# Performance work log

Measured on AMD Instinct MI355X. Metric: run time of the kernel, lower is better.

## Reference

```python
import jax, jax.numpy as jnp
import numpy as np

N = 100000   # nodes
E = 1600000  # edges
IN = 128     # in_dim
H = 64       # hidden_dim
EPS = 1e-5


def layer_norm(x, g, b):
    mu = x.mean(-1, keepdims=True)
    v = ((x - mu) ** 2).mean(-1, keepdims=True)
    return (x - mu) * jax.lax.rsqrt(v + EPS) * g + b


def gcn_conv(x, W, b, src, dst, dinv):
    # PyG GCNConv: x' = D^{-1/2}(A+I)D^{-1/2} X W + b (degrees include self-loops)
    h = x @ W                                   # [N, H]
    coef = dinv[src] * dinv[dst]                # [E]
    agg = jax.ops.segment_sum(h[src] * coef[:, None], dst, num_segments=N)
    agg = agg + h * (dinv * dinv)[:, None]      # self-loop term
    return agg + b


def setup_inputs() -> dict:
    key = jax.random.key(0)
    ks = jax.random.split(key, 12)
    inp = {
        "x": jax.random.normal(ks[0], (N, IN), jnp.float32),
        "edge_index": jax.random.randint(ks[1], (2, E), 0, N, dtype=jnp.int64
                                         if jax.config.jax_enable_x64 else jnp.int32),
    }
    dims = [(IN, H), (H, H), (H, H)]
    for i, (di, do) in enumerate(dims, start=1):
        inp[f"W{i}"] = jax.random.normal(ks[2 * i], (di, do), jnp.float32) / np.sqrt(di)
        inp[f"b{i}"] = jnp.zeros((do,), jnp.float32)
        inp[f"g{i}"] = jnp.ones((do,), jnp.float32)
        inp[f"be{i}"] = jnp.zeros((do,), jnp.float32)
    inp["Wh"] = jax.random.normal(ks[11], (H, 1), jnp.float32) / np.sqrt(H)
    inp["bh"] = jnp.zeros((1,), jnp.float32)
    return inp


def reference(x, edge_index, W1, b1, g1, be1, W2, b2, g2, be2, W3, b3, g3, be3, Wh, bh):
    src, dst = edge_index[0], edge_index[1]
    deg = jax.ops.segment_sum(jnp.ones((E,), x.dtype), dst, num_segments=N) + 1.0
    dinv = jax.lax.rsqrt(deg)
    for W, b, g, be in ((W1, b1, g1, be1), (W2, b2, g2, be2), (W3, b3, g3, be3)):
        x = gcn_conv(x, W, b, src, dst, dinv)
        x = layer_norm(x, g, be)
        x = jax.nn.gelu(x, approximate=False)  # F.gelu default = exact erf
        # dropout omitted (eval mode / deterministic reference)
    return (x @ Wh + bh).squeeze(-1)  # [N]
```

## Files before the change

### kernel.cpp

```cpp
#include <hip/hip_runtime.h>
#include <math.h>

#define NODES 100000
#define EDGES 1600000
#define NBUCK 196
#define BCAP2 12288
#define EPB 4096
#define BINB 391
#define GEMMB 1563

typedef __attribute__((ext_vector_type(8))) short short8;
typedef __attribute__((ext_vector_type(4))) float floatx4;
typedef __attribute__((ext_vector_type(4))) unsigned uv4;

__device__ __forceinline__ float gsum8(float x) {
#pragma unroll
  for (int o = 4; o > 0; o >>= 1) x += __shfl_xor(x, o, 64);
  return x;
}

__device__ __forceinline__ short f2bf(float f) {
  union { float f; unsigned u; } v;
  v.f = f;
  unsigned r = 0x7fffu + ((v.u >> 16) & 1u);
  return (short)((v.u + r) >> 16);
}
__device__ __forceinline__ float bflo(unsigned p) {
  union { unsigned u; float f; } v; v.u = p << 16; return v.f;
}
__device__ __forceinline__ float bfhi(unsigned p) {
  union { unsigned u; float f; } v; v.u = p & 0xffff0000u; return v.f;
}

#define BIN_SMEM (4 * 256 * 4 + EPB * 4 + EPB)
__device__ __forceinline__ void bin_body(char* smemraw, int b, const int* __restrict__ src,
                                         const int* __restrict__ dst, int* __restrict__ bins,
                                         int* __restrict__ gcur) {
  int* cnt = (int*)smemraw;
  int* gb = cnt + 256;
  int* lb = gb + 256;
  int* lcur = lb + 256;
  int* rec = lcur + 256;
  unsigned char* rbk = (unsigned char*)(rec + EPB);
  int t = threadIdx.x;
  cnt[t] = 0;
  __syncthreads();
  int base = b * EPB;
  int nv = EDGES - base; if (nv > EPB) nv = EPB;
  int s[16], d[16];
#pragma unroll
  for (int j = 0; j < 16; ++j) {
    int e = base + j * 256 + t;
    if (e < EDGES) {
      s[j] = src[e];
      d[j] = dst[e];
      atomicAdd(&cnt[d[j] >> 9], 1);
    } else {
      d[j] = -1;
    }
  }
  __syncthreads();
  int c = cnt[t];
  lb[t] = c;
  __syncthreads();
  for (int o = 1; o < 256; o <<= 1) {
    int u = (t >= o) ? lb[t - o] : 0;
    __syncthreads();
    lb[t] += u;
    __syncthreads();
  }
  int ex = lb[t] - c;
  gb[t] = (c > 0) ? atomicAdd(&gcur[t], c) : 0;
  __syncthreads();
  lb[t] = ex;
  lcur[t] = ex;
  __syncthreads();
#pragma unroll
  for (int j = 0; j < 16; ++j) {
    if (d[j] >= 0) {
      int bk = d[j] >> 9;
      int lp = atomicAdd(&lcur[bk], 1);
      rec[lp] = s[j] | ((d[j] & 511) << 17);
      rbk[lp] = (unsigned char)bk;
    }
  }
  __syncthreads();
  for (int i = t; i < nv; i += 256) {
    int bk = rbk[i];
    int pos = gb[bk] + (i - lb[bk]);
    if (pos < BCAP2) bins[bk * BCAP2 + pos] = rec[i];
  }
}

#define FILL_SMEM (256 * 4 + 512 * 4 + 512 * 4 + 4 * 4 + BCAP2 * 4)
__device__ __forceinline__ void fill_body(char* smemraw, int b, const int* __restrict__ bins,
                                          const int* __restrict__ gcur, int* __restrict__ rowptr,
                                          float* __restrict__ dinv, int* __restrict__ csr) {
  int* bsm = (int*)smemraw;
  int* cnt = bsm + 256;
  int* cur = cnt + 512;
  int* wtot = cur + 512;
  int* stage = wtot + 4;
  int t = threadIdx.x;
  int v = 0;
  if (t < NBUCK) { v = gcur[t]; if (v > BCAP2) v = BCAP2; }
  bsm[t] = v;
  cnt[t] = 0; cnt[t + 256] = 0;
  __syncthreads();
  for (int o = 1; o < 256; o <<= 1) {
    int u = (t >= o) ? bsm[t - o] : 0;
    __syncthreads();
    bsm[t] += u;
    __syncthreads();
  }
  if (b == 0 && t == NBUCK - 1) rowptr[NODES] = bsm[t];
  int cb = gcur[b]; if (cb > BCAP2) cb = BCAP2;
  int bbase = bsm[b] - cb;
  const int* bp = &bins[(size_t)b * BCAP2];
  for (int i = t; i < cb; i += 256)
    atomicAdd(&cnt[(bp[i] >> 17) & 511], 1);
  __syncthreads();
  int a0 = cnt[2 * t], a1 = cnt[2 * t + 1];
  int sum2 = a0 + a1;
  int lane = t & 63, w = t >> 6;
  int inc = sum2;
#pragma unroll
  for (int o = 1; o < 64; o <<= 1) {
    int u = __shfl_up(inc, o, 64);
    if (lane >= o) inc += u;
  }
  if (lane == 63) wtot[w] = inc;
  __syncthreads();
  int wpre = 0;
  for (int ww = 0; ww < w; ++ww) wpre += wtot[ww];
  int l0 = wpre + inc - sum2;
  int l1 = l0 + a0;
  int n0 = b * 512 + 2 * t, n1 = n0 + 1;
  if (n0 < NODES) { rowptr[n0] = bbase + l0; dinv[n0] = rsqrtf((float)a0 + 1.0f); }
  if (n1 < NODES) { rowptr[n1] = bbase + l1; dinv[n1] = rsqrtf((float)a1 + 1.0f); }
  cur[2 * t] = l0; cur[2 * t + 1] = l1;
  __syncthreads();
  for (int i = t; i < cb; i += 256) {
    int pk = bp[i];
    int lp = atomicAdd(&cur[(pk >> 17) & 511], 1);
    stage[lp] = pk & 0x1FFFF;
  }
  __syncthreads();
  for (int i = t; i < cb; i += 256) csr[bbase + i] = stage[i];
}

#define GEMM_SMEM (64 * 136 * 2)
__device__ __forceinline__ void gemm_body(char* smemraw, int tile0, const float* __restrict__ x,
                                          const float* __restrict__ W, short* __restrict__ hs) {
  constexpr int K = 128, KP = K + 8;
  short* wt = (short*)smemraw;
  for (int idx = threadIdx.x; idx < K * 64; idx += 256) {
    int k = idx >> 6, n = idx & 63;
    wt[n * KP + k] = f2bf(W[idx]);
  }
  __syncthreads();
  int wid = threadIdx.x >> 6, lane = threadIdx.x & 63;
  int tile = tile0 + wid;
  if (tile * 16 >= NODES) return;
  int m = lane & 15, q = lane >> 4;

  short8 bfr[4][K / 32];
#pragma unroll
  for (int ct = 0; ct < 4; ++ct)
#pragma unroll
    for (int ks = 0; ks < K / 32; ++ks)
      bfr[ct][ks] = *reinterpret_cast<const short8*>(&wt[(ct * 16 + m) * KP + ks * 32 + q * 8]);

  floatx4 acc[4];
#pragma unroll
  for (int ct = 0; ct < 4; ++ct) acc[ct] = {0.f, 0.f, 0.f, 0.f};
  int r0 = tile * 16;
#pragma unroll
  for (int ks = 0; ks < K / 32; ++ks) {
    const float* xp = &x[(size_t)(r0 + m) * K + ks * 32 + q * 8];
    floatx4 a0 = *reinterpret_cast<const floatx4*>(xp);
    floatx4 a1 = *reinterpret_cast<const floatx4*>(xp + 4);
    short8 af;
#pragma unroll
    for (int j = 0; j < 4; ++j) { af[j] = f2bf(a0[j]); af[4 + j] = f2bf(a1[j]); }
#pragma unroll
    for (int ct = 0; ct < 4; ++ct)
      acc[ct] = __builtin_amdgcn_mfma_f32_16x16x32_bf16(af, bfr[ct][ks], acc[ct], 0, 0, 0);
  }
#pragma unroll
  for (int ct = 0; ct < 4; ++ct)
#pragma unroll
    for (int r = 0; r < 4; ++r) {
      int row = r0 + q * 4 + r, col = ct * 16 + m;
      hs[row * 64 + col] = f2bf(acc[ct][r]);
    }
}

template <bool PRESCALED>
__device__ __forceinline__ void do_agg(const uv4* __restrict__ hsv, const float* __restrict__ dinv,
                                       const int* __restrict__ csr, int n, int e0, int e1,
                                       int lane, float dn, float acc[8]) {
  int q = lane & 7, srcb = lane & 0x38;
  uv4 sv = hsv[(size_t)n * 8 + q];
#pragma unroll
  for (int w = 0; w < 4; ++w) {
    float lo = bflo(sv[w]), hi = bfhi(sv[w]);
    if constexpr (PRESCALED) { acc[2 * w] = lo; acc[2 * w + 1] = hi; }
    else { acc[2 * w] = lo * dn; acc[2 * w + 1] = hi * dn; }
  }
  for (int base = e0; base < e1; base += 8) {
    int cnt = e1 - base;
    if (cnt > 8) cnt = 8;
    int a = base + (q < cnt ? q : 0);
    int sidx = csr[a];
    float gq = 1.0f;
    if constexpr (!PRESCALED) gq = dinv[sidx];
    int s[8]; float wj[8];
#pragma unroll
    for (int j = 0; j < 8; ++j) {
      s[j] = __shfl(sidx, srcb | j, 64);
      if constexpr (!PRESCALED) {
        float bj = __shfl(gq, srcb | j, 64);
        wj[j] = (j < cnt) ? bj : 0.0f;
      } else {
        wj[j] = 1.0f;
      }
    }
    uv4 v[8];
#pragma unroll
    for (int j = 0; j < 8; ++j) v[j] = hsv[(size_t)s[j] * 8 + q];
    if constexpr (PRESCALED) {
      if (cnt == 8) {
#pragma unroll
        for (int j = 0; j < 8; ++j)
#pragma unroll
          for (int w = 0; w < 4; ++w) { acc[2 * w] += bflo(v[j][w]); acc[2 * w + 1] += bfhi(v[j][w]); }
      } else {
#pragma unroll
        for (int j = 0; j < 8; ++j)
          if (j < cnt)
#pragma unroll
            for (int w = 0; w < 4; ++w) { acc[2 * w] += bflo(v[j][w]); acc[2 * w + 1] += bfhi(v[j][w]); }
      }
    } else {
#pragma unroll
      for (int j = 0; j < 8; ++j)
#pragma unroll
        for (int w = 0; w < 4; ++w) {
          acc[2 * w]     += wj[j] * bflo(v[j][w]);
          acc[2 * w + 1] += wj[j] * bfhi(v[j][w]);
        }
    }
  }
}

template <bool PRESCALED>
__global__ __launch_bounds__(256) void k_aggg(const short* __restrict__ hs,
                                              const float* __restrict__ dinv,
                                              const int* __restrict__ rowptr,
                                              const int* __restrict__ csr,
                                              const float* __restrict__ bias,
                                              const float* __restrict__ gam,
                                              const float* __restrict__ bet,
                                              const float* __restrict__ W,
                                              short* __restrict__ hsn) {
  __shared__ __align__(16) short wt[64 * 72];
  __shared__ __align__(16) short ut[32 * 72];
  int t = threadIdx.x;
  for (int idx = t; idx < 4096; idx += 256) {
    int k = idx >> 6, n = idx & 63;
    wt[n * 72 + k] = f2bf(W[idx]);
  }
  const uv4* hsv = (const uv4*)hs;
  int lane = t & 63, wid = t >> 6;
  int g = lane >> 3, q = lane & 7;
  int nb0 = blockIdx.x * 32;
  int r = wid * 8 + g;
  int n = nb0 + r;
  int e0 = rowptr[n], e1 = rowptr[n + 1];
  float dn = dinv[n];
  float acc[8];
  do_agg<PRESCALED>(hsv, dinv, csr, n, e0, e1, lane, dn, acc);

  const floatx4* bi4 = (const floatx4*)bias;
  floatx4 b0 = bi4[q * 2], b1 = bi4[q * 2 + 1];
#pragma unroll
  for (int f = 0; f < 4; ++f) { acc[f] = acc[f] * dn + b0[f]; acc[f + 4] = acc[f + 4] * dn + b1[f]; }

  float lsum = 0.f;
#pragma unroll
  for (int f = 0; f < 8; ++f) lsum += acc[f];
  float mu = gsum8(lsum) * (1.0f / 64.0f);
  float d[8], lvar = 0.f;
#pragma unroll
  for (int f = 0; f < 8; ++f) { d[f] = acc[f] - mu; lvar += d[f] * d[f]; }
  float rs = rsqrtf(gsum8(lvar) * (1.0f / 64.0f) + 1e-5f);
  const floatx4* gm4 = (const floatx4*)gam;
  const floatx4* bt4 = (const floatx4*)bet;
  floatx4 g0 = gm4[q * 2], g1 = gm4[q * 2 + 1];
  floatx4 t0 = bt4[q * 2], t1 = bt4[q * 2 + 1];
  short8 us;
#pragma unroll
  for (int f = 0; f < 8; ++f) {
    float gv = (f < 4) ? g0[f] : g1[f - 4];
    float tv = (f < 4) ? t0[f] : t1[f - 4];
    float vv = d[f] * rs * gv + tv;
    float u = 0.5f * vv * (1.0f + erff(vv * 0.70710678118654752f));
    us[f] = f2bf(u * dn);
  }
  *reinterpret_cast<short8*>(&ut[r * 72 + q * 8]) = us;
  __syncthreads();

  int m = lane & 15, q2 = lane >> 4;
  int tile = wid >> 1, cb = (wid & 1) * 2;
  short8 bfr[2][2];
#pragma unroll
  for (int ct = 0; ct < 2; ++ct)
#pragma unroll
    for (int ks = 0; ks < 2; ++ks)
      bfr[ct][ks] = *reinterpret_cast<const short8*>(&wt[((cb + ct) * 16 + m) * 72 + ks * 32 + q2 * 8]);
  floatx4 ac[2];
#pragma unroll
  for (int ct = 0; ct < 2; ++ct) ac[ct] = {0.f, 0.f, 0.f, 0.f};
#pragma unroll
  for (int ks = 0; ks < 2; ++ks) {
    short8 af = *reinterpret_cast<const short8*>(&ut[(tile * 16 + m) * 72 + ks * 32 + q2 * 8]);
#pragma unroll
    for (int ct = 0; ct < 2; ++ct)
      ac[ct] = __builtin_amdgcn_mfma_f32_16x16x32_bf16(af, bfr[ct][ks], ac[ct], 0, 0, 0);
  }
#pragma unroll
  for (int ct = 0; ct < 2; ++ct)
#pragma unroll
    for (int rr = 0; rr < 4; ++rr) {
      int row = nb0 + tile * 16 + q2 * 4 + rr, col = (cb + ct) * 16 + m;
      hsn[row * 64 + col] = f2bf(ac[ct][rr]);
    }
}

__global__ __launch_bounds__(256) void k_agg_fin(const short* __restrict__ hs,
                                                 const float* __restrict__ dinv,
                                                 const int* __restrict__ rowptr,
                                                 const int* __restrict__ csr,
                                                 const float* __restrict__ bias,
                                                 const float* __restrict__ gam,
                                                 const float* __restrict__ bet,
                                                 const float* __restrict__ Wh,
                                                 const float* __restrict__ bh,
                                                 float* __restrict__ out) {
  const uv4* hsv = (const uv4*)hs;
  int lane = threadIdx.x & 63, wid = threadIdx.x >> 6;
  int g = lane >> 3, q = lane & 7;
  int n = blockIdx.x * 32 + wid * 8 + g;
  int e0 = rowptr[n], e1 = rowptr[n + 1];
  float dn = dinv[n];
  float acc[8];
  do_agg<true>(hsv, dinv, csr, n, e0, e1, lane, dn, acc);
  const floatx4* bi4 = (const floatx4*)bias;
  floatx4 b0 = bi4[q * 2], b1 = bi4[q * 2 + 1];
#pragma unroll
  for (int f = 0; f < 4; ++f) { acc[f] = acc[f] * dn + b0[f]; acc[f + 4] = acc[f + 4] * dn + b1[f]; }
  float lsum = 0.f;
#pragma unroll
  for (int f = 0; f < 8; ++f) lsum += acc[f];
  float mu = gsum8(lsum) * (1.0f / 64.0f);
  float d[8], lvar = 0.f;
#pragma unroll
  for (int f = 0; f < 8; ++f) { d[f] = acc[f] - mu; lvar += d[f] * d[f]; }
  float rs = rsqrtf(gsum8(lvar) * (1.0f / 64.0f) + 1e-5f);
  const floatx4* gm4 = (const floatx4*)gam;
  const floatx4* bt4 = (const floatx4*)bet;
  floatx4 g0 = gm4[q * 2], g1 = gm4[q * 2 + 1];
  floatx4 t0 = bt4[q * 2], t1 = bt4[q * 2 + 1];
  const floatx4* wh4 = (const floatx4*)Wh;
  floatx4 w0 = wh4[q * 2], w1 = wh4[q * 2 + 1];
  float lp = 0.f;
#pragma unroll
  for (int f = 0; f < 8; ++f) {
    float gv = (f < 4) ? g0[f] : g1[f - 4];
    float tv = (f < 4) ? t0[f] : t1[f - 4];
    float wv = (f < 4) ? w0[f] : w1[f - 4];
    float vv = d[f] * rs * gv + tv;
    float u = 0.5f * vv * (1.0f + erff(vv * 0.70710678118654752f));
    lp += u * wv;
  }
  float p = gsum8(lp);
  if (q == 0) out[n] = p + bh[0];
}

__global__ __launch_bounds__(256) void k_pre1(const int* __restrict__ src, const int* __restrict__ dst,
                                              int* __restrict__ bins, int* __restrict__ gcur,
                                              const float* __restrict__ x, const float* __restrict__ W1,
                                              short* __restrict__ hs) {
  __shared__ __align__(16) char smem[BIN_SMEM];
  int b = blockIdx.x;
  if (b < BINB) bin_body(smem, b, src, dst, bins, gcur);
  else gemm_body(smem, (b - BINB) * 4, x, W1, hs);
}

__global__ __launch_bounds__(256) void k_pre2(const int* __restrict__ bins, const int* __restrict__ gcur,
                                              int* __restrict__ rowptr, float* __restrict__ dinv,
                                              int* __restrict__ csr) {
  __shared__ __align__(16) char smem[FILL_SMEM];
  fill_body(smem, blockIdx.x, bins, gcur, rowptr, dinv, csr);
}

__global__ __launch_bounds__(256) void k_bin2(const int* src, const int* dst, int* bins, int* gcur) {
  __shared__ __align__(16) char smem[BIN_SMEM];
  bin_body(smem, blockIdx.x, src, dst, bins, gcur);
}
__global__ __launch_bounds__(256) void k_fillb2(const int* bins, const int* gcur, int* rowptr,
                                                float* dinv, int* csr) {
  __shared__ __align__(16) char smem[FILL_SMEM];
  fill_body(smem, blockIdx.x, bins, gcur, rowptr, dinv, csr);
}
__global__ __launch_bounds__(256) void k_gemm(const float* x, const float* W, short* hs) {
  __shared__ __align__(16) char smem[GEMM_SMEM];
  gemm_body(smem, blockIdx.x * 4, x, W, hs);
}

extern "C" void kernel_launch(void* const* d_in, const int* in_sizes, int n_in,
                              void* d_out, int out_size, void* d_ws, size_t ws_size,
                              hipStream_t stream) {
  const float* x  = (const float*)d_in[0];
  const int* ei   = (const int*)d_in[1];
  const float* W1 = (const float*)d_in[2];
  const float* b1 = (const float*)d_in[3];
  const float* g1 = (const float*)d_in[4];
  const float* be1= (const float*)d_in[5];
  const float* W2 = (const float*)d_in[6];
  const float* b2 = (const float*)d_in[7];
  const float* g2 = (const float*)d_in[8];
  const float* be2= (const float*)d_in[9];
  const float* W3 = (const float*)d_in[10];
  const float* b3 = (const float*)d_in[11];
  const float* g3 = (const float*)d_in[12];
  const float* be3= (const float*)d_in[13];
  const float* Wh = (const float*)d_in[14];
  const float* bh = (const float*)d_in[15];
  const int* srcp = ei;
  const int* dstp = ei + EDGES;

  char* ws = (char*)d_ws;
  size_t off = 0;
  auto take = [&](size_t bytes) {
    char* p = ws + off;
    off = (off + bytes + 255) & ~(size_t)255;
    return p;
  };
  float* dinv = (float*)take((size_t)NODES * 4);
  int* rowptr = (int*)take((size_t)(NODES + 1) * 4);
  int* csr    = (int*)take((size_t)EDGES * 4);
  short* hs_a = (short*)take((size_t)NODES * 64 * 2);
  short* hs_b = (short*)take((size_t)NODES * 64 * 2);

  size_t bins_sz = (size_t)NBUCK * BCAP2 * 4;
  bool overlap = (ws_size >= off + bins_sz + 4096);
  int* bins; int* gcur;
  if (overlap) {
    bins = (int*)take(bins_sz);
    gcur = (int*)take((size_t)NBUCK * 4);
  } else {
    bins = (int*)hs_a;
    gcur = (int*)hs_b;
  }

  (void)hipMemsetAsync(gcur, 0, (size_t)NBUCK * 4, stream);
  if (overlap) {
    k_pre1<<<BINB + GEMMB, 256, 0, stream>>>(srcp, dstp, bins, gcur, x, W1, hs_a);
    k_pre2<<<NBUCK, 256, 0, stream>>>(bins, gcur, rowptr, dinv, csr);
  } else {
    k_bin2<<<BINB, 256, 0, stream>>>(srcp, dstp, bins, gcur);
    k_fillb2<<<NBUCK, 256, 0, stream>>>(bins, gcur, rowptr, dinv, csr);
    k_gemm<<<GEMMB, 256, 0, stream>>>(x, W1, hs_a);
  }
  k_aggg<false><<<NODES / 32, 256, 0, stream>>>(hs_a, dinv, rowptr, csr, b1, g1, be1, W2, hs_b);
  k_aggg<true><<<NODES / 32, 256, 0, stream>>>(hs_b, dinv, rowptr, csr, b2, g2, be2, W3, hs_a);
  k_agg_fin<<<NODES / 32, 256, 0, stream>>>(hs_a, dinv, rowptr, csr, b3, g3, be3, Wh, bh, (float*)d_out);
}
```

Before: 265.3 us.

## Sort nodes by in-degree within buckets to balance aggregation warps

```diff
diff --git a/kernel.cpp b/kernel.cpp
--- a/kernel.cpp
+++ b/kernel.cpp
@@ -92,20 +92,24 @@
   }
 }
 
-#define FILL_SMEM (256 * 4 + 512 * 4 + 512 * 4 + 4 * 4 + BCAP2 * 4)
+#define FILL_SMEM ((256 + 512 + 512 + 4 + BCAP2 + 128) * 4)
 __device__ __forceinline__ void fill_body(char* smemraw, int b, const int* __restrict__ bins,
                                           const int* __restrict__ gcur, int* __restrict__ rowptr,
-                                          float* __restrict__ dinv, int* __restrict__ csr) {
+                                          float* __restrict__ dinv, int* __restrict__ csr,
+                                          int* __restrict__ perm) {
   int* bsm = (int*)smemraw;
   int* cnt = bsm + 256;
   int* cur = cnt + 512;
   int* wtot = cur + 512;
   int* stage = wtot + 4;
+  int* hist = stage + BCAP2;
+  int* hbase = hist + 64;
   int t = threadIdx.x;
   int v = 0;
   if (t < NBUCK) { v = gcur[t]; if (v > BCAP2) v = BCAP2; }
   bsm[t] = v;
   cnt[t] = 0; cnt[t + 256] = 0;
+  if (t < 64) hist[t] = 0;
   __syncthreads();
   for (int o = 1; o < 256; o <<= 1) {
     int u = (t >= o) ? bsm[t - o] : 0;
@@ -121,6 +125,10 @@
     atomicAdd(&cnt[(bp[i] >> 17) & 511], 1);
   __syncthreads();
   int a0 = cnt[2 * t], a1 = cnt[2 * t + 1];
+  int n0 = b * 512 + 2 * t, n1 = n0 + 1;
+  int d0 = a0 > 63 ? 63 : a0, d1 = a1 > 63 ? 63 : a1;
+  if (n0 < NODES) atomicAdd(&hist[d0], 1);
+  if (n1 < NODES) atomicAdd(&hist[d1], 1);
   int sum2 = a0 + a1;
   int lane = t & 63, w = t >> 6;
   int inc = sum2;
@@ -135,16 +143,27 @@
   for (int ww = 0; ww < w; ++ww) wpre += wtot[ww];
   int l0 = wpre + inc - sum2;
   int l1 = l0 + a0;
-  int n0 = b * 512 + 2 * t, n1 = n0 + 1;
   if (n0 < NODES) { rowptr[n0] = bbase + l0; dinv[n0] = rsqrtf((float)a0 + 1.0f); }
   if (n1 < NODES) { rowptr[n1] = bbase + l1; dinv[n1] = rsqrtf((float)a1 + 1.0f); }
   cur[2 * t] = l0; cur[2 * t + 1] = l1;
+  if (t < 64) {
+    int h = hist[t];
+    int hinc = h;
+#pragma unroll
+    for (int o = 1; o < 64; o <<= 1) {
+      int u = __shfl_up(hinc, o, 64);
+      if (lane >= o) hinc += u;
+    }
+    hbase[t] = hinc - h;
+  }
   __syncthreads();
   for (int i = t; i < cb; i += 256) {
     int pk = bp[i];
     int lp = atomicAdd(&cur[(pk >> 17) & 511], 1);
     stage[lp] = pk & 0x1FFFF;
   }
+  if (n0 < NODES) { int r0p = atomicAdd(&hbase[d0], 1); perm[b * 512 + r0p] = n0; }
+  if (n1 < NODES) { int r1p = atomicAdd(&hbase[d1], 1); perm[b * 512 + r1p] = n1; }
   __syncthreads();
   for (int i = t; i < cb; i += 256) csr[bbase + i] = stage[i];
 }
@@ -259,6 +278,7 @@
                                               const float* __restrict__ dinv,
                                               const int* __restrict__ rowptr,
                                               const int* __restrict__ csr,
+                                              const int* __restrict__ perm,
                                               const float* __restrict__ bias,
                                               const float* __restrict__ gam,
                                               const float* __restrict__ bet,
@@ -276,7 +296,7 @@
   int g = lane >> 3, q = lane & 7;
   int nb0 = blockIdx.x * 32;
   int r = wid * 8 + g;
-  int n = nb0 + r;
+  int n = perm[nb0 + r];
   int e0 = rowptr[n], e1 = rowptr[n + 1];
   float dn = dinv[n];
   float acc[8];
@@ -333,7 +353,8 @@
   for (int ct = 0; ct < 2; ++ct)
 #pragma unroll
     for (int rr = 0; rr < 4; ++rr) {
-      int row = nb0 + tile * 16 + q2 * 4 + rr, col = (cb + ct) * 16 + m;
+      int row = perm[nb0 + tile * 16 + q2 * 4 + rr];
+      int col = (cb + ct) * 16 + m;
       hsn[row * 64 + col] = f2bf(ac[ct][rr]);
     }
 }
@@ -342,6 +363,7 @@
                                                  const float* __restrict__ dinv,
                                                  const int* __restrict__ rowptr,
                                                  const int* __restrict__ csr,
+                                                 const int* __restrict__ perm,
                                                  const float* __restrict__ bias,
                                                  const float* __restrict__ gam,
                                                  const float* __restrict__ bet,
@@ -351,7 +373,7 @@
   const uv4* hsv = (const uv4*)hs;
   int lane = threadIdx.x & 63, wid = threadIdx.x >> 6;
   int g = lane >> 3, q = lane & 7;
-  int n = blockIdx.x * 32 + wid * 8 + g;
+  int n = perm[blockIdx.x * 32 + wid * 8 + g];
   int e0 = rowptr[n], e1 = rowptr[n + 1];
   float dn = dinv[n];
   float acc[8];
@@ -400,9 +422,9 @@
 
 __global__ __launch_bounds__(256) void k_pre2(const int* __restrict__ bins, const int* __restrict__ gcur,
                                               int* __restrict__ rowptr, float* __restrict__ dinv,
-                                              int* __restrict__ csr) {
+                                              int* __restrict__ csr, int* __restrict__ perm) {
   __shared__ __align__(16) char smem[FILL_SMEM];
-  fill_body(smem, blockIdx.x, bins, gcur, rowptr, dinv, csr);
+  fill_body(smem, blockIdx.x, bins, gcur, rowptr, dinv, csr, perm);
 }
 
 __global__ __launch_bounds__(256) void k_bin2(const int* src, const int* dst, int* bins, int* gcur) {
@@ -410,9 +432,9 @@
   bin_body(smem, blockIdx.x, src, dst, bins, gcur);
 }
 __global__ __launch_bounds__(256) void k_fillb2(const int* bins, const int* gcur, int* rowptr,
-                                                float* dinv, int* csr) {
+                                                float* dinv, int* csr, int* perm) {
   __shared__ __align__(16) char smem[FILL_SMEM];
-  fill_body(smem, blockIdx.x, bins, gcur, rowptr, dinv, csr);
+  fill_body(smem, blockIdx.x, bins, gcur, rowptr, dinv, csr, perm);
 }
 __global__ __launch_bounds__(256) void k_gemm(const float* x, const float* W, short* hs) {
   __shared__ __align__(16) char smem[GEMM_SMEM];
@@ -451,6 +473,7 @@
   float* dinv = (float*)take((size_t)NODES * 4);
   int* rowptr = (int*)take((size_t)(NODES + 1) * 4);
   int* csr    = (int*)take((size_t)EDGES * 4);
+  int* perm   = (int*)take((size_t)NODES * 4);
   short* hs_a = (short*)take((size_t)NODES * 64 * 2);
   short* hs_b = (short*)take((size_t)NODES * 64 * 2);
 
@@ -468,13 +491,13 @@
   (void)hipMemsetAsync(gcur, 0, (size_t)NBUCK * 4, stream);
   if (overlap) {
     k_pre1<<<BINB + GEMMB, 256, 0, stream>>>(srcp, dstp, bins, gcur, x, W1, hs_a);
-    k_pre2<<<NBUCK, 256, 0, stream>>>(bins, gcur, rowptr, dinv, csr);
+    k_pre2<<<NBUCK, 256, 0, stream>>>(bins, gcur, rowptr, dinv, csr, perm);
   } else {
     k_bin2<<<BINB, 256, 0, stream>>>(srcp, dstp, bins, gcur);
-    k_fillb2<<<NBUCK, 256, 0, stream>>>(bins, gcur, rowptr, dinv, csr);
+    k_fillb2<<<NBUCK, 256, 0, stream>>>(bins, gcur, rowptr, dinv, csr, perm);
     k_gemm<<<GEMMB, 256, 0, stream>>>(x, W1, hs_a);
   }
-  k_aggg<false><<<NODES / 32, 256, 0, stream>>>(hs_a, dinv, rowptr, csr, b1, g1, be1, W2, hs_b);
-  k_aggg<true><<<NODES / 32, 256, 0, stream>>>(hs_b, dinv, rowptr, csr, b2, g2, be2, W3, hs_a);
-  k_agg_fin<<<NODES / 32, 256, 0, stream>>>(hs_a, dinv, rowptr, csr, b3, g3, be3, Wh, bh, (float*)d_out);
-}
+  k_aggg<false><<<NODES / 32, 256, 0, stream>>>(hs_a, dinv, rowptr, csr, perm, b1, g1, be1, W2, hs_b);
+  k_aggg<true><<<NODES / 32, 256, 0, stream>>>(hs_b, dinv, rowptr, csr, perm, b2, g2, be2, W3, hs_a);
+  k_agg_fin<<<NODES / 32, 256, 0, stream>>>(hs_a, dinv, rowptr, csr, perm, b3, g3, be3, Wh, bh, (float*)d_out);
+}
```

Result: slower. 279.4 us (+5.3%).

## Use 16 lanes per node in aggregation kernels with 8-byte gathers

Applied to the files above, without the earlier changes.

```diff
diff --git a/kernel.cpp b/kernel.cpp
--- a/kernel.cpp
+++ b/kernel.cpp
@@ -12,10 +12,11 @@
 typedef __attribute__((ext_vector_type(8))) short short8;
 typedef __attribute__((ext_vector_type(4))) float floatx4;
 typedef __attribute__((ext_vector_type(4))) unsigned uv4;
-
-__device__ __forceinline__ float gsum8(float x) {
-#pragma unroll
-  for (int o = 4; o > 0; o >>= 1) x += __shfl_xor(x, o, 64);
+typedef __attribute__((ext_vector_type(2))) unsigned uv2;
+
+__device__ __forceinline__ float gsum16(float x) {
+#pragma unroll
+  for (int o = 8; o > 0; o >>= 1) x += __shfl_xor(x, o, 64);
   return x;
 }
 
@@ -30,6 +31,11 @@
 }
 __device__ __forceinline__ float bfhi(unsigned p) {
   union { unsigned u; float f; } v; v.u = p & 0xffff0000u; return v.f;
+}
+__device__ __forceinline__ unsigned pack2(float a, float b) {
+  unsigned lo = (unsigned)(unsigned short)f2bf(a);
+  unsigned hi = (unsigned)(unsigned short)f2bf(b);
+  return lo | (hi << 16);
 }
 
 #define BIN_SMEM (4 * 256 * 4 + EPB * 4 + EPB)
@@ -197,27 +203,27 @@
 }
 
 template <bool PRESCALED>
-__device__ __forceinline__ void do_agg(const uv4* __restrict__ hsv, const float* __restrict__ dinv,
+__device__ __forceinline__ void do_agg(const uv2* __restrict__ hsv, const float* __restrict__ dinv,
                                        const int* __restrict__ csr, int n, int e0, int e1,
-                                       int lane, float dn, float acc[8]) {
-  int q = lane & 7, srcb = lane & 0x38;
-  uv4 sv = hsv[(size_t)n * 8 + q];
-#pragma unroll
-  for (int w = 0; w < 4; ++w) {
+                                       int lane, float dn, float acc[4]) {
+  int q = lane & 15, srcb = lane & 0x30;
+  uv2 sv = hsv[(size_t)n * 16 + q];
+#pragma unroll
+  for (int w = 0; w < 2; ++w) {
     float lo = bflo(sv[w]), hi = bfhi(sv[w]);
     if constexpr (PRESCALED) { acc[2 * w] = lo; acc[2 * w + 1] = hi; }
     else { acc[2 * w] = lo * dn; acc[2 * w + 1] = hi * dn; }
   }
-  for (int base = e0; base < e1; base += 8) {
+  for (int base = e0; base < e1; base += 16) {
     int cnt = e1 - base;
-    if (cnt > 8) cnt = 8;
+    if (cnt > 16) cnt = 16;
     int a = base + (q < cnt ? q : 0);
     int sidx = csr[a];
     float gq = 1.0f;
     if constexpr (!PRESCALED) gq = dinv[sidx];
-    int s[8]; float wj[8];
-#pragma unroll
-    for (int j = 0; j < 8; ++j) {
+    int s[16]; float wj[16];
+#pragma unroll
+    for (int j = 0; j < 16; ++j) {
       s[j] = __shfl(sidx, srcb | j, 64);
       if constexpr (!PRESCALED) {
         float bj = __shfl(gq, srcb | j, 64);
@@ -226,27 +232,27 @@
         wj[j] = 1.0f;
       }
     }
-    uv4 v[8];
-#pragma unroll
-    for (int j = 0; j < 8; ++j) v[j] = hsv[(size_t)s[j] * 8 + q];
+    uv2 v[16];
+#pragma unroll
+    for (int j = 0; j < 16; ++j) v[j] = hsv[(size_t)s[j] * 16 + q];
     if constexpr (PRESCALED) {
-      if (cnt == 8) {
-#pragma unroll
-        for (int j = 0; j < 8; ++j)
-#pragma unroll
-          for (int w = 0; w < 4; ++w) { acc[2 * w] += bflo(v[j][w]); acc[2 * w + 1] += bfhi(v[j][w]); }
+      if (cnt == 16) {
+#pragma unroll
+        for (int j = 0; j < 16; ++j)
+#pragma unroll
+          for (int w = 0; w < 2; ++w) { acc[2 * w] += bflo(v[j][w]); acc[2 * w + 1] += bfhi(v[j][w]); }
       } else {
 #pragma unroll
-        for (int j = 0; j < 8; ++j)
+        for (int j = 0; j < 16; ++j)
           if (j < cnt)
 #pragma unroll
-            for (int w = 0; w < 4; ++w) { acc[2 * w] += bflo(v[j][w]); acc[2 * w + 1] += bfhi(v[j][w]); }
+            for (int w = 0; w < 2; ++w) { acc[2 * w] += bflo(v[j][w]); acc[2 * w + 1] += bfhi(v[j][w]); }
       }
     } else {
 #pragma unroll
-      for (int j = 0; j < 8; ++j)
-#pragma unroll
-        for (int w = 0; w < 4; ++w) {
+      for (int j = 0; j < 16; ++j)
+#pragma unroll
+        for (int w = 0; w < 2; ++w) {
           acc[2 * w]     += wj[j] * bflo(v[j][w]);
           acc[2 * w + 1] += wj[j] * bfhi(v[j][w]);
         }
@@ -265,77 +271,66 @@
                                               const float* __restrict__ W,
                                               short* __restrict__ hsn) {
   __shared__ __align__(16) short wt[64 * 72];
-  __shared__ __align__(16) short ut[32 * 72];
+  __shared__ __align__(16) short ut[16 * 72];
   int t = threadIdx.x;
   for (int idx = t; idx < 4096; idx += 256) {
     int k = idx >> 6, n = idx & 63;
     wt[n * 72 + k] = f2bf(W[idx]);
   }
-  const uv4* hsv = (const uv4*)hs;
+  const uv2* hsv = (const uv2*)hs;
   int lane = t & 63, wid = t >> 6;
-  int g = lane >> 3, q = lane & 7;
-  int nb0 = blockIdx.x * 32;
-  int r = wid * 8 + g;
+  int g = lane >> 4, q = lane & 15;
+  int nb0 = blockIdx.x * 16;
+  int r = wid * 4 + g;
   int n = nb0 + r;
   int e0 = rowptr[n], e1 = rowptr[n + 1];
   float dn = dinv[n];
-  float acc[8];
+  float acc[4];
   do_agg<PRESCALED>(hsv, dinv, csr, n, e0, e1, lane, dn, acc);
 
   const floatx4* bi4 = (const floatx4*)bias;
-  floatx4 b0 = bi4[q * 2], b1 = bi4[q * 2 + 1];
-#pragma unroll
-  for (int f = 0; f < 4; ++f) { acc[f] = acc[f] * dn + b0[f]; acc[f + 4] = acc[f + 4] * dn + b1[f]; }
-
-  float lsum = 0.f;
-#pragma unroll
-  for (int f = 0; f < 8; ++f) lsum += acc[f];
-  float mu = gsum8(lsum) * (1.0f / 64.0f);
-  float d[8], lvar = 0.f;
-#pragma unroll
-  for (int f = 0; f < 8; ++f) { d[f] = acc[f] - mu; lvar += d[f] * d[f]; }
-  float rs = rsqrtf(gsum8(lvar) * (1.0f / 64.0f) + 1e-5f);
+  floatx4 b0 = bi4[q];
+#pragma unroll
+  for (int f = 0; f < 4; ++f) acc[f] = acc[f] * dn + b0[f];
+
+  float lsum = acc[0] + acc[1] + acc[2] + acc[3];
+  float mu = gsum16(lsum) * (1.0f / 64.0f);
+  float d[4], lvar = 0.f;
+#pragma unroll
+  for (int f = 0; f < 4; ++f) { d[f] = acc[f] - mu; lvar += d[f] * d[f]; }
+  float rs = rsqrtf(gsum16(lvar) * (1.0f / 64.0f) + 1e-5f);
   const floatx4* gm4 = (const floatx4*)gam;
   const floatx4* bt4 = (const floatx4*)bet;
-  floatx4 g0 = gm4[q * 2], g1 = gm4[q * 2 + 1];
-  floatx4 t0 = bt4[q * 2], t1 = bt4[q * 2 + 1];
-  short8 us;
-#pragma unroll
-  for (int f = 0; f < 8; ++f) {
-    float gv = (f < 4) ? g0[f] : g1[f - 4];
-    float tv = (f < 4) ? t0[f] : t1[f - 4];
-    float vv = d[f] * rs * gv + tv;
-    float u = 0.5f * vv * (1.0f + erff(vv * 0.70710678118654752f));
-    us[f] = f2bf(u * dn);
-  }
-  *reinterpret_cast<short8*>(&ut[r * 72 + q * 8]) = us;
+  floatx4 g0 = gm4[q];
+  floatx4 t0 = bt4[q];
+  float u[4];
+#pragma unroll
+  for (int f = 0; f < 4; ++f) {
+    float vv = d[f] * rs * g0[f] + t0[f];
+    u[f] = 0.5f * vv * (1.0f + erff(vv * 0.70710678118654752f)) * dn;
+  }
+  uv2 us;
+  us[0] = pack2(u[0], u[1]);
+  us[1] = pack2(u[2], u[3]);
+  *reinterpret_cast<uv2*>(&ut[r * 72 + q * 4]) = us;
   __syncthreads();
 
   int m = lane & 15, q2 = lane >> 4;
-  int tile = wid >> 1, cb = (wid & 1) * 2;
-  short8 bfr[2][2];
-#pragma unroll
-  for (int ct = 0; ct < 2; ++ct)
-#pragma unroll
-    for (int ks = 0; ks < 2; ++ks)
-      bfr[ct][ks] = *reinterpret_cast<const short8*>(&wt[((cb + ct) * 16 + m) * 72 + ks * 32 + q2 * 8]);
-  floatx4 ac[2];
-#pragma unroll
-  for (int ct = 0; ct < 2; ++ct) ac[ct] = {0.f, 0.f, 0.f, 0.f};
+  short8 bfr[2];
+#pragma unroll
+  for (int ks = 0; ks < 2; ++ks)
+    bfr[ks] = *reinterpret_cast<const short8*>(&wt[(wid * 16 + m) * 72 + ks * 32 + q2 * 8]);
+  floatx4 ac = {0.f, 0.f, 0.f, 0.f};
 #pragma unroll
   for (int ks = 0; ks < 2; ++ks) {
-    short8 af = *reinterpret_cast<const short8*>(&ut[(tile * 16 + m) * 72 + ks * 32 + q2 * 8]);
-#pragma unroll
-    for (int ct = 0; ct < 2; ++ct)
-      ac[ct] = __builtin_amdgcn_mfma_f32_16x16x32_bf16(af, bfr[ct][ks], ac[ct], 0, 0, 0);
-  }
-#pragma unroll
-  for (int ct = 0; ct < 2; ++ct)
-#pragma unroll
-    for (int rr = 0; rr < 4; ++rr) {
-      int row = nb0 + tile * 16 + q2 * 4 + rr, col = (cb + ct) * 16 + m;
-      hsn[row * 64 + col] = f2bf(ac[ct][rr]);
-    }
+    short8 af = *reinterpret_cast<const short8*>(&ut[m * 72 + ks * 32 + q2 * 8]);
+    ac = __builtin_amdgcn_mfma_f32_16x16x32_bf16(af, bfr[ks], ac, 0, 0, 0);
+  }
+#pragma unroll
+  for (int rr = 0; rr < 4; ++rr) {
+    int row = nb0 + q2 * 4 + rr, col = wid * 16 + m;
+    hsn[row * 64 + col] = f2bf(ac[rr]);
+  }
 }
 
 __global__ __launch_bounds__(256) void k_agg_fin(const short* __restrict__ hs,
@@ -348,43 +343,38 @@
                                                  const float* __restrict__ Wh,
                                                  const float* __restrict__ bh,
                                                  float* __restrict__ out) {
-  const uv4* hsv = (const uv4*)hs;
+  const uv2* hsv = (const uv2*)hs;
   int lane = threadIdx.x & 63, wid = threadIdx.x >> 6;
-  int g = lane >> 3, q = lane & 7;
-  int n = blockIdx.x * 32 + wid * 8 + g;
+  int g = lane >> 4, q = lane & 15;
+  int n = blockIdx.x * 16 + wid * 4 + g;
   int e0 = rowptr[n], e1 = rowptr[n + 1];
   float dn = dinv[n];
-  float acc[8];
+  float acc[4];
   do_agg<true>(hsv, dinv, csr, n, e0, e1, lane, dn, acc);
   const floatx4* bi4 = (const floatx4*)bias;
-  floatx4 b0 = bi4[q * 2], b1 = bi4[q * 2 + 1];
-#pragma unroll
-  for (int f = 0; f < 4; ++f) { acc[f] = acc[f] * dn + b0[f]; acc[f + 4] = acc[f + 4] * dn + b1[f]; }
-  float lsum = 0.f;
-#pragma unroll
-  for (int f = 0; f < 8; ++f) lsum += acc[f];
-  float mu = gsum8(lsum) * (1.0f / 64.0f);
-  float d[8], lvar = 0.f;
-#pragma unroll
-  for (int f = 0; f < 8; ++f) { d[f] = acc[f] - mu; lvar += d[f] * d[f]; }
-  float rs = rsqrtf(gsum8(lvar) * (1.0f / 64.0f) + 1e-5f);
+  floatx4 b0 = bi4[q];
+#pragma unroll
+  for (int f = 0; f < 4; ++f) acc[f] = acc[f] * dn + b0[f];
+  float lsum = acc[0] + acc[1] + acc[2] + acc[3];
+  float mu = gsum16(lsum) * (1.0f / 64.0f);
+  float d[4], lvar = 0.f;
+#pragma unroll
+  for (int f = 0; f < 4; ++f) { d[f] = acc[f] - mu; lvar += d[f] * d[f]; }
+  float rs = rsqrtf(gsum16(lvar) * (1.0f / 64.0f) + 1e-5f);
   const floatx4* gm4 = (const floatx4*)gam;
   const floatx4* bt4 = (const floatx4*)bet;
-  floatx4 g0 = gm4[q * 2], g1 = gm4[q * 2 + 1];
-  floatx4 t0 = bt4[q * 2], t1 = bt4[q * 2 + 1];
+  floatx4 g0 = gm4[q];
+  floatx4 t0 = bt4[q];
   const floatx4* wh4 = (const floatx4*)Wh;
-  floatx4 w0 = wh4[q * 2], w1 = wh4[q * 2 + 1];
+  floatx4 w0 = wh4[q];
   float lp = 0.f;
 #pragma unroll
-  for (int f = 0; f < 8; ++f) {
-    float gv = (f < 4) ? g0[f] : g1[f - 4];
-    float tv = (f < 4) ? t0[f] : t1[f - 4];
-    float wv = (f < 4) ? w0[f] : w1[f - 4];
-    float vv = d[f] * rs * gv + tv;
-    float u = 0.5f * vv * (1.0f + erff(vv * 0.70710678118654752f));
-    lp += u * wv;
-  }
-  float p = gsum8(lp);
+  for (int f = 0; f < 4; ++f) {
+    float vv = d[f] * rs * g0[f] + t0[f];
+    float uu = 0.5f * vv * (1.0f + erff(vv * 0.70710678118654752f));
+    lp += uu * w0[f];
+  }
+  float p = gsum16(lp);
   if (q == 0) out[n] = p + bh[0];
 }
 
@@ -474,7 +464,7 @@
     k_fillb2<<<NBUCK, 256, 0, stream>>>(bins, gcur, rowptr, dinv, csr);
     k_gemm<<<GEMMB, 256, 0, stream>>>(x, W1, hs_a);
   }
-  k_aggg<false><<<NODES / 32, 256, 0, stream>>>(hs_a, dinv, rowptr, csr, b1, g1, be1, W2, hs_b);
-  k_aggg<true><<<NODES / 32, 256, 0, stream>>>(hs_b, dinv, rowptr, csr, b2, g2, be2, W3, hs_a);
-  k_agg_fin<<<NODES / 32, 256, 0, stream>>>(hs_a, dinv, rowptr, csr, b3, g3, be3, Wh, bh, (float*)d_out);
-}
+  k_aggg<false><<<NODES / 16, 256, 0, stream>>>(hs_a, dinv, rowptr, csr, b1, g1, be1, W2, hs_b);
+  k_aggg<true><<<NODES / 16, 256, 0, stream>>>(hs_b, dinv, rowptr, csr, b2, g2, be2, W3, hs_a);
+  k_agg_fin<<<NODES / 16, 256, 0, stream>>>(hs_a, dinv, rowptr, csr, b3, g3, be3, Wh, bh, (float*)d_out);
+}
```

After: 281.8 us. 1.06x slower.
